# Kernel tuning notes

Measured on AMD Instinct MI355X. Metric: run time of the kernel, lower is better.

## Reference

```python
import jax, jax.numpy as jnp
import numpy as np


def setup_inputs() -> dict:
    key = jax.random.key(0)
    ks = jax.random.split(key, 8)
    B, S, V, E, H = 64, 512, 50257, 512, 1024
    scale1 = 1.0 / np.sqrt(E + H)
    scale2 = 1.0 / np.sqrt(H + E)
    return {
        "sequence": jax.random.randint(ks[0], (B, S), 0, V, dtype=jnp.int64),
        "init_h1": jax.random.uniform(ks[1], (B, H), jnp.float32, -0.1, 0.1),
        "init_h2": jax.random.uniform(ks[2], (B, E), jnp.float32, -0.1, 0.1),
        "emb_W": jax.random.normal(ks[3], (V, E), jnp.float32) * 0.02,
        "W1": jax.random.normal(ks[4], (E + H, H), jnp.float32) * scale1,
        "b1": jnp.zeros((H,), jnp.float32),
        "W2": jax.random.normal(ks[5], (H + E, E), jnp.float32) * scale2,
        "b2": jnp.zeros((E,), jnp.float32),
        "out_b": jnp.zeros((V,), jnp.float32),
    }


def reference(sequence, init_h1, init_h2, emb_W, W1, b1, W2, b2, out_b):
    # embeddings: [B, S, E] -> scan over time axis
    emb = emb_W[sequence]  # gather, [B, S, E]
    emb_t = jnp.swapaxes(emb, 0, 1)  # [S, B, E]

    def step(carry, token):
        h1, h2 = carry  # [B,H], [B,E]
        in1 = jnp.concatenate([token, h1], axis=1)  # [B, E+H]
        new_h1 = jnp.tanh(in1 @ W1 + b1)            # [B, H]
        in2 = jnp.concatenate([new_h1, h2], axis=1)  # [B, H+E]
        new_h2 = jnp.tanh(in2 @ W2 + b2)             # [B, E]
        return (new_h1, new_h2), None

    (h1, h2), _ = jax.lax.scan(step, (init_h1, init_h2), emb_t)
    # tied output projection: Linear with weight = embedding table [V, E]
    probabilities = h2 @ emb_W.T + out_b  # [B, V]
    return probabilities, h1, h2
```

## Files before the change

kernel.cpp:

```cpp
#include <hip/hip_runtime.h>
#include <hip/hip_bf16.h>

#define BB 64
#define EE 512
#define HH 1024
#define KK 1536
#define VV 50257
#define SS 512

#define NWG1 64
#define NWG2 32
#define NWG (NWG1 + NWG2)
#define RING 8
#define PADU 32

typedef __bf16 bf16x8 __attribute__((ext_vector_type(8)));
typedef float f32x4 __attribute__((ext_vector_type(4)));

__device__ __forceinline__ bf16x8 load_bf8(const __bf16* p) {
    return *reinterpret_cast<const bf16x8*>(p);
}

__device__ __forceinline__ bf16x8 cvt8(const float* p) {
    f32x4 a = *reinterpret_cast<const f32x4*>(p);
    f32x4 b = *reinterpret_cast<const f32x4*>(p + 4);
    bf16x8 r;
    r[0] = (__bf16)a[0]; r[1] = (__bf16)a[1]; r[2] = (__bf16)a[2]; r[3] = (__bf16)a[3];
    r[4] = (__bf16)b[0]; r[5] = (__bf16)b[1]; r[6] = (__bf16)b[2]; r[7] = (__bf16)b[3];
    return r;
}

__device__ __forceinline__ void st16c(void* p, f32x4 v) {
    asm volatile("global_store_dwordx4 %0, %1, off sc0 sc1" :: "v"(p), "v"(v) : "memory");
}
__device__ __forceinline__ f32x4 ld16c(const void* p) {
    f32x4 r;
    asm volatile("global_load_dwordx4 %0, %1, off sc0 sc1" : "=v"(r) : "v"(p) : "memory");
    return r;
}
union cvu { f32x4 f; bf16x8 h8; __bf16 h[8]; };

__device__ __forceinline__ void wwait(const unsigned* slots, int nslots, unsigned target) {
    const int l = threadIdx.x & 63;
    const int idx = l < nslots ? l : 0;
    for (;;) {
        unsigned v = __hip_atomic_load(&slots[idx * PADU], __ATOMIC_RELAXED,
                                       __HIP_MEMORY_SCOPE_AGENT);
        if (l >= nslots) v = target;
        if (__all((int)(v >= target))) break;
        __builtin_amdgcn_s_sleep(1);
    }
    asm volatile("" ::: "memory");
}

__device__ __forceinline__ unsigned minpoll(const unsigned* slots, int nslots) {
    const int l = threadIdx.x & 63;
    unsigned v = 0xFFFFFFFFu;
    if (l < nslots)
        v = __hip_atomic_load(&slots[l * PADU], __ATOMIC_RELAXED,
                              __HIP_MEMORY_SCOPE_AGENT);
    #pragma unroll
    for (int o = 32; o; o >>= 1) {
        unsigned u = (unsigned)__shfl_xor((int)v, o, 64);
        v = u < v ? u : v;
    }
    return v;
}

__device__ __forceinline__ void wsignal(unsigned* slot, unsigned val) {
    asm volatile("s_waitcnt vmcnt(0)" ::: "memory");
    if ((threadIdx.x & 63) == 0)
        __hip_atomic_store(slot, val, __ATOMIC_RELAXED, __HIP_MEMORY_SCOPE_AGENT);
}

__device__ __forceinline__ float ftanh(float x) {
    float ax = fabsf(x);
    float e = __expf(-2.0f * ax);
    float r = (1.0f - e) / (1.0f + e);
    return x < 0.0f ? -r : r;
}

__global__ void tokens_kernel(const void* __restrict__ seq, int* __restrict__ tok,
                              unsigned* __restrict__ bar) {
    int z = blockIdx.x * 256 + threadIdx.x;
    if (z < 4 * 96 * PADU)
        __hip_atomic_store(&bar[z], 0u, __ATOMIC_RELAXED, __HIP_MEMORY_SCOPE_AGENT);
    const unsigned* u = (const unsigned*)seq;
    bool is64 = true;
    #pragma unroll 1
    for (int i = 0; i < 64; ++i) {
        if (u[2 * i + 1] != 0u) { is64 = false; break; }
    }
    int i = blockIdx.x * 256 + threadIdx.x;
    if (i < BB * SS) tok[i] = is64 ? (int)u[2 * i] : (int)u[i];
}

__global__ __launch_bounds__(256) void transpose_kernel(
    const float* __restrict__ in, __bf16* __restrict__ out, int R, int C) {
    __shared__ float t[32][33];
    int bc = C >> 5;
    int br = blockIdx.x / bc;
    int bco = blockIdx.x % bc;
    int R0 = br << 5, C0 = bco << 5;
    int c = threadIdx.x & 31, r0 = threadIdx.x >> 5;
    #pragma unroll
    for (int i = 0; i < 4; ++i) {
        int r = r0 + i * 8;
        t[r][c] = in[(size_t)(R0 + r) * C + C0 + c];
    }
    __syncthreads();
    #pragma unroll
    for (int i = 0; i < 4; ++i) {
        int r = r0 + i * 8;
        out[(size_t)(C0 + r) * R + R0 + c] = (__bf16)t[c][r];
    }
}

__global__ void init_kernel(const float* __restrict__ h1, const float* __restrict__ h2,
                            __bf16* __restrict__ h1bf, __bf16* __restrict__ h2bf) {
    int i = blockIdx.x * 256 + threadIdx.x;
    if (i < BB * HH) h1bf[i] = (__bf16)h1[i];
    if (i < BB * EE) h2bf[i] = (__bf16)h2[i];
}

__global__ __launch_bounds__(256, 1) void rnn_persist3(
    const int* __restrict__ tok32, const float* __restrict__ embW,
    const float* __restrict__ b1, const float* __restrict__ b2,
    const __bf16* __restrict__ W1t, const __bf16* __restrict__ W2t,
    __bf16* __restrict__ h1r, __bf16* __restrict__ h2r,
    float* __restrict__ h1out, float* __restrict__ h2out,
    unsigned* __restrict__ bar) {
    const int bid = blockIdx.x;
    const bool g1 = bid < NWG1;
    const int rb = g1 ? bid : bid - NWG1;
    const int mi = rb & 3;
    const int ni = rb >> 2;
    const int m0 = mi << 4;
    const int n0 = ni << 6;
    const int tid = threadIdx.x;
    const int w = tid >> 6;
    const int l = tid & 63;
    const int l16 = l & 15;
    const int kg = l >> 4;
    unsigned* f1s = bar + mi * (96 * PADU);
    unsigned* f2s = f1s + 64 * PADU;
    unsigned* myf = g1 ? &f1s[(ni * 4 + w) * PADU] : &f2s[(ni * 4 + w) * PADU];

    __shared__ int tok_s[SS][16];
    __shared__ float red[2][4][16][68];

    if (g1) {
        for (int idx = tid; idx < SS * 16; idx += 256) {
            int t = idx >> 4, r = idx & 15;
            tok_s[t][r] = tok32[(m0 + r) * SS + t];
        }
    }

    const __bf16* Wt = g1 ? W1t : W2t;
    bf16x8 wreg[12][4];
    #pragma unroll
    for (int t = 0; t < 12; ++t) {
        const int kb = 32 * (w + 4 * t) + kg * 8;
        #pragma unroll
        for (int nf = 0; nf < 4; ++nf)
            wreg[t][nf] = load_bf8(Wt + (size_t)(n0 + nf * 16 + l16) * KK + kb);
    }
    {
        f32x4* p1 = reinterpret_cast<f32x4*>(&wreg[0][0]);
        #pragma unroll
        for (int q = 0; q < 48; ++q) asm volatile("" : "+v"(p1[q]));
    }

    const int r1 = 4 * w + ((l & 31) >> 3);
    const int c1 = (l & 7) * 8;
    const float* bias = g1 ? b1 : b2;
    const f32x4 blo = *reinterpret_cast<const f32x4*>(bias + n0 + c1);
    const f32x4 bhi = *reinterpret_cast<const f32x4*>(bias + n0 + c1 + 4);

    unsigned f2c = 0;

    __syncthreads();

    if (g1) {
        for (int i = 0; i < SS; ++i) {
            const __bf16* h1i = h1r + (size_t)(i & 7) * BB * HH;
            __bf16*       h1n = h1r + (size_t)((i + 1) & 7) * BB * HH;

            f32x4 acc[4] = {{0,0,0,0},{0,0,0,0},{0,0,0,0},{0,0,0,0}};
            const float* er = embW + (size_t)tok_s[i][l16] * EE;
            #pragma unroll
            for (int t = 0; t < 4; ++t) {
                bf16x8 ae = cvt8(er + 32 * (w + 4 * t) + kg * 8);
                #pragma unroll
                for (int nf = 0; nf < 4; ++nf)
                    acc[nf] = __builtin_amdgcn_mfma_f32_16x16x32_bf16(
                        ae, wreg[t][nf], acc[nf], 0, 0, 0);
            }
            __builtin_amdgcn_sched_barrier(0);

            if (i >= 7 && (int)f2c < i - 7) {
                do { f2c = minpoll(f2s, 32); } while ((int)f2c < i - 7);
            }

            if (i) wwait(f1s, 64, (unsigned)i);

            const __bf16* h1row = h1i + (m0 + l16) * HH;
            bf16x8 ah[8];
            #pragma unroll
            for (int u = 0; u < 8; ++u) {
                cvu t_; t_.f = ld16c(h1row + 32 * (w + 4 * u) + kg * 8);
                ah[u] = t_.h8;
            }
            asm volatile("s_waitcnt vmcnt(0)" ::: "memory");
            __builtin_amdgcn_sched_barrier(0);

            #pragma unroll
            for (int u = 0; u < 8; ++u)
                #pragma unroll
                for (int nf = 0; nf < 4; ++nf)
                    acc[nf] = __builtin_amdgcn_mfma_f32_16x16x32_bf16(
                        ah[u], wreg[u + 4][nf], acc[nf], 0, 0, 0);

            #pragma unroll
            for (int nf = 0; nf < 4; ++nf)
                #pragma unroll
                for (int q = 0; q < 4; ++q)
                    red[i & 1][w][kg * 4 + q][nf * 16 + l16] = acc[nf][q];
            __syncthreads();

            if ((l & 63) < 32) {
                f32x4 lo = blo, hi = bhi;
                #pragma unroll
                for (int p = 0; p < 4; ++p) {
                    lo += *reinterpret_cast<const f32x4*>(&red[i & 1][p][r1][c1]);
                    hi += *reinterpret_cast<const f32x4*>(&red[i & 1][p][r1][c1 + 4]);
                }
                cvu o;
                #pragma unroll
                for (int j = 0; j < 4; ++j) {
                    o.h[j]     = (__bf16)ftanh(lo[j]);
                    o.h[j + 4] = (__bf16)ftanh(hi[j]);
                }
                st16c(h1n + (m0 + r1) * HH + n0 + c1, o.f);
                if (i == SS - 1) {
                    float* op = h1out + (m0 + r1) * HH + n0 + c1;
                    #pragma unroll
                    for (int j = 0; j < 8; ++j)
                        op[j] = __bfloat162float(((__hip_bfloat16*)&o.h[j])[0]);
                }
            }
            wsignal(myf, (unsigned)(i + 1));
        }
    } else {
        for (int j = 1; j <= SS; ++j) {
            const __bf16* h1j = h1r + (size_t)(j & 7) * BB * HH;
            const __bf16* h2p = h2r + (size_t)((j - 1) & 7) * BB * EE;
            __bf16*       h2n = h2r + (size_t)(j & 7) * BB * EE;

            wwait(f1s, 64, (unsigned)j);
            const __bf16* h1row = h1j + (m0 + l16) * HH;
            bf16x8 ah[8];
            #pragma unroll
            for (int t = 0; t < 8; ++t) {
                cvu t_; t_.f = ld16c(h1row + 32 * (w + 4 * t) + kg * 8);
                ah[t] = t_.h8;
            }
            if (j >= 2) wwait(f2s, 32, (unsigned)(j - 1));
            const __bf16* h2row = h2p + (m0 + l16) * EE;
            bf16x8 a2[4];
            #pragma unroll
            for (int u = 0; u < 4; ++u) {
                cvu t_; t_.f = ld16c(h2row + 32 * (w + 4 * u) + kg * 8);
                a2[u] = t_.h8;
            }
            asm volatile("s_waitcnt vmcnt(0)" ::: "memory");
            __builtin_amdgcn_sched_barrier(0);

            f32x4 acc[4] = {{0,0,0,0},{0,0,0,0},{0,0,0,0},{0,0,0,0}};
            #pragma unroll
            for (int t = 0; t < 8; ++t)
                #pragma unroll
                for (int nf = 0; nf < 4; ++nf)
                    acc[nf] = __builtin_amdgcn_mfma_f32_16x16x32_bf16(
                        ah[t], wreg[t][nf], acc[nf], 0, 0, 0);
            #pragma unroll
            for (int u = 0; u < 4; ++u)
                #pragma unroll
                for (int nf = 0; nf < 4; ++nf)
                    acc[nf] = __builtin_amdgcn_mfma_f32_16x16x32_bf16(
                        a2[u], wreg[u + 8][nf], acc[nf], 0, 0, 0);

            #pragma unroll
            for (int nf = 0; nf < 4; ++nf)
                #pragma unroll
                for (int q = 0; q < 4; ++q)
                    red[j & 1][w][kg * 4 + q][nf * 16 + l16] = acc[nf][q];
            __syncthreads();

            if ((l & 63) < 32) {
                f32x4 lo = blo, hi = bhi;
                #pragma unroll
                for (int p = 0; p < 4; ++p) {
                    lo += *reinterpret_cast<const f32x4*>(&red[j & 1][p][r1][c1]);
                    hi += *reinterpret_cast<const f32x4*>(&red[j & 1][p][r1][c1 + 4]);
                }
                cvu o;
                #pragma unroll
                for (int q = 0; q < 4; ++q) {
                    o.h[q]     = (__bf16)ftanh(lo[q]);
                    o.h[q + 4] = (__bf16)ftanh(hi[q]);
                }
                st16c(h2n + (m0 + r1) * EE + n0 + c1, o.f);
                if (j == SS) {
                    float* op = h2out + (m0 + r1) * EE + n0 + c1;
                    #pragma unroll
                    for (int q = 0; q < 8; ++q)
                        op[q] = __bfloat162float(((__hip_bfloat16*)&o.h[q])[0]);
                }
            }
            wsignal(myf, (unsigned)j);
        }
    }
}

__global__ __launch_bounds__(256) void step_kernel(
    const int* __restrict__ tok32,
    const float* __restrict__ embW,
    const float* __restrict__ b1, const float* __restrict__ b2,
    const __bf16* __restrict__ W1t, const __bf16* __restrict__ W2t,
    const __bf16* __restrict__ h1cur, __bf16* __restrict__ h1next,
    const __bf16* __restrict__ h2cur, __bf16* __restrict__ h2next,
    float* __restrict__ h1f32, float* __restrict__ h2f32,
    int t, int g1, int g2) {
    const int bid = blockIdx.x;
    const bool is1 = bid < 128;
    if (is1 ? (g1 == 0) : (g2 == 0)) return;
    const int rb = is1 ? bid : (bid - 128);
    const int mi = rb & 3;
    const int ni = rb >> 2;
    const int m0 = mi << 4;
    const int n0 = ni << 5;
    const int N = is1 ? HH : EE;
    const int tid = threadIdx.x;
    const int w = tid >> 6;
    const int l = tid & 63;
    const int l16 = l & 15;
    const int kg = l >> 4;

    __shared__ int tok_s[16];
    __shared__ float red[4][16][33];

    if (is1 && tid < 16) tok_s[tid] = tok32[(m0 + tid) * SS + t];
    __syncthreads();

    const __bf16* Wt = is1 ? W1t : W2t;
    f32x4 acc0 = {0.f, 0.f, 0.f, 0.f};
    f32x4 acc1 = {0.f, 0.f, 0.f, 0.f};
    const int row = m0 + l16;
    const int kb = w * 384;

    #pragma unroll 4
    for (int kk = 0; kk < 384; kk += 32) {
        const int k = kb + kk + kg * 8;
        bf16x8 a;
        if (is1) {
            if (k < EE) a = cvt8(embW + (size_t)tok_s[l16] * EE + k);
            else        a = load_bf8(h1cur + row * HH + (k - EE));
        } else {
            if (k < HH) a = load_bf8(h1cur + row * HH + k);
            else        a = load_bf8(h2cur + row * EE + (k - HH));
        }
        bf16x8 bf0 = load_bf8(Wt + (size_t)(n0 + l16) * KK + k);
        bf16x8 bf1 = load_bf8(Wt + (size_t)(n0 + 16 + l16) * KK + k);
        acc0 = __builtin_amdgcn_mfma_f32_16x16x32_bf16(a, bf0, acc0, 0, 0, 0);
        acc1 = __builtin_amdgcn_mfma_f32_16x16x32_bf16(a, bf1, acc1, 0, 0, 0);
    }

    #pragma unroll
    for (int i = 0; i < 4; ++i) {
        red[w][kg * 4 + i][l16]      = acc0[i];
        red[w][kg * 4 + i][16 + l16] = acc1[i];
    }
    __syncthreads();

    const float* bias = is1 ? b1 : b2;
    for (int c = tid; c < 512; c += 256) {
        int m = c >> 5, n = c & 31;
        float s = red[0][m][n] + red[1][m][n] + red[2][m][n] + red[3][m][n];
        s = tanhf(s + bias[n0 + n]);
        int gi = (m0 + m) * N + (n0 + n);
        if (is1) {
            h1next[gi] = (__bf16)s;
            if (h1f32) h1f32[gi] = s;
        } else {
            h2next[gi] = (__bf16)s;
            if (h2f32) h2f32[gi] = s;
        }
    }
}

__global__ __launch_bounds__(256) void proj_kernel(
    const __bf16* __restrict__ h2bf,
    const float* __restrict__ embW,
    const float* __restrict__ outb,
    float* __restrict__ out) {
    const int v0 = blockIdx.x << 6;
    const int tid = threadIdx.x;
    const int w = tid >> 6;
    const int l = tid & 63;
    const int l16 = l & 15, kg = l >> 4;
    const int vcol = v0 + w * 16 + l16;
    const int vr = vcol < VV ? vcol : VV - 1;
    f32x4 acc[4] = {{0,0,0,0},{0,0,0,0},{0,0,0,0},{0,0,0,0}};
    #pragma unroll 2
    for (int k0 = 0; k0 < EE; k0 += 32) {
        const int k = k0 + kg * 8;
        bf16x8 bfr = cvt8(embW + (size_t)vr * EE + k);
        #pragma unroll
        for (int mf = 0; mf < 4; ++mf) {
            bf16x8 a = load_bf8(h2bf + (mf * 16 + l16) * EE + k);
            acc[mf] = __builtin_amdgcn_mfma_f32_16x16x32_bf16(a, bfr, acc[mf], 0, 0, 0);
        }
    }
    if (vcol < VV) {
        const float bb = outb[vcol];
        #pragma unroll
        for (int mf = 0; mf < 4; ++mf) {
            #pragma unroll
            for (int i = 0; i < 4; ++i) {
                int b = mf * 16 + kg * 4 + i;
                out[(size_t)b * VV + vcol] = acc[mf][i] + bb;
            }
        }
    }
}

extern "C" void kernel_launch(void* const* d_in, const int* in_sizes, int n_in,
                              void* d_out, int out_size, void* d_ws, size_t ws_size,
                              hipStream_t stream) {
    const void* seq      = d_in[0];
    const float* init_h1 = (const float*)d_in[1];
    const float* init_h2 = (const float*)d_in[2];
    const float* embW    = (const float*)d_in[3];
    const float* W1      = (const float*)d_in[4];
    const float* b1      = (const float*)d_in[5];
    const float* W2      = (const float*)d_in[6];
    const float* b2      = (const float*)d_in[7];
    const float* outb    = (const float*)d_in[8];
    float* out = (float*)d_out;

    char* ws = (char*)d_ws;
    int* tok = (int*)ws;                 ws += (size_t)BB * SS * 4;
    __bf16* W1t = (__bf16*)ws;           ws += (size_t)HH * KK * 2;
    __bf16* W2t = (__bf16*)ws;           ws += (size_t)EE * KK * 2;
    __bf16* h1r = (__bf16*)ws;           ws += (size_t)RING * BB * HH * 2;
    __bf16* h2r = (__bf16*)ws;           ws += (size_t)RING * BB * EE * 2;
    unsigned* bar = (unsigned*)ws;       ws += (size_t)4 * 96 * PADU * 4;

    hipLaunchKernelGGL(tokens_kernel, dim3(128), dim3(256), 0, stream, seq, tok, bar);
    hipLaunchKernelGGL(transpose_kernel, dim3((KK / 32) * (HH / 32)), dim3(256), 0, stream,
                       W1, W1t, KK, HH);
    hipLaunchKernelGGL(transpose_kernel, dim3((KK / 32) * (EE / 32)), dim3(256), 0, stream,
                       W2, W2t, KK, EE);
    hipLaunchKernelGGL(init_kernel, dim3(256), dim3(256), 0, stream,
                       init_h1, init_h2, h1r, h2r);

    float* h1out = out + (size_t)BB * VV;
    float* h2out = h1out + (size_t)BB * HH;

    const int* tok_c = tok;
    const __bf16* W1t_c = W1t;
    const __bf16* W2t_c = W2t;
    void* args[] = {
        (void*)&tok_c, (void*)&embW, (void*)&b1, (void*)&b2,
        (void*)&W1t_c, (void*)&W2t_c,
        (void*)&h1r, (void*)&h2r,
        (void*)&h1out, (void*)&h2out, (void*)&bar
    };
    hipError_t err = hipLaunchCooperativeKernel((void*)rnn_persist3, dim3(NWG), dim3(256),
                                                args, 0, stream);
    if (err != hipSuccess) {
        __bf16* h1bf[2] = {h1r, h1r + (size_t)BB * HH};
        __bf16* h2bf[2] = {h2r, h2r + (size_t)BB * EE};
        for (int t = 0; t <= SS; ++t) {
            int g1 = (t < SS) ? 1 : 0;
            int g2 = (t >= 1) ? 1 : 0;
            const __bf16* h1cur = h1bf[t & 1];
            __bf16* h1next      = h1bf[(t + 1) & 1];
            const __bf16* h2cur = h2bf[(t + 1) & 1];
            __bf16* h2next      = h2bf[t & 1];
            float* h1f = (t == SS - 1) ? h1out : nullptr;
            float* h2f = (t == SS) ? h2out : nullptr;
            hipLaunchKernelGGL(step_kernel, dim3(192), dim3(256), 0, stream,
                               tok, embW, b1, b2, W1t, W2t,
                               h1cur, h1next, h2cur, h2next, h1f, h2f, t, g1, g2);
        }
    }

    hipLaunchKernelGGL(proj_kernel, dim3((VV + 63) / 64), dim3(256), 0, stream,
                       h2r, embW, outb, out);
}
```

Baseline: 2.120 ms.

## Replace flag barriers with step-tagged hidden-state messages for fine-grained dataflow sync

Each bf16 pair of hidden state is now stored with its timestep tag in a 64-bit word. Consumers spin on the data itself until every tag matches, so the per-wave flag stores, the vmcnt drain before signalling and the separate flag polling are gone. This is meant to cut the latency of the serial recurrent chain at each step. The cost is twice the memory traffic for hidden-state reads and writes, extra clear and init kernels, and guard-bounded spin loops that could fall through and read stale data.

```diff
diff --git a/kernel.cpp b/kernel.cpp
--- a/kernel.cpp
+++ b/kernel.cpp
@@ -11,11 +11,16 @@
 #define NWG1 64
 #define NWG2 32
 #define NWG (NWG1 + NWG2)
-#define RING 8
 #define PADU 32
+#define GUARD_MAX 8192
 
 typedef __bf16 bf16x8 __attribute__((ext_vector_type(8)));
 typedef float f32x4 __attribute__((ext_vector_type(4)));
+typedef unsigned u32x2 __attribute__((ext_vector_type(2)));
+typedef unsigned long long u64;
+
+union frg { unsigned u[4]; bf16x8 h; };
+union pk2 { __bf16 h[2]; unsigned u; };
 
 __device__ __forceinline__ bf16x8 load_bf8(const __bf16* p) {
     return *reinterpret_cast<const bf16x8*>(p);
@@ -30,27 +35,17 @@
     return r;
 }
 
-__device__ __forceinline__ void st16c(void* p, f32x4 v) {
-    asm volatile("global_store_dwordx4 %0, %1, off sc0 sc1" :: "v"(p), "v"(v) : "memory");
-}
-__device__ __forceinline__ f32x4 ld16c(const void* p) {
-    f32x4 r;
-    asm volatile("global_load_dwordx4 %0, %1, off sc0 sc1" : "=v"(r) : "v"(p) : "memory");
+template<int OFF>
+__device__ __forceinline__ u32x2 ld8o(const void* p) {
+    u32x2 r;
+    asm volatile("global_load_dwordx2 %0, %1, off offset:%2 sc0 sc1"
+                 : "=v"(r) : "v"(p), "i"(OFF));
     return r;
 }
-union cvu { f32x4 f; bf16x8 h8; __bf16 h[8]; };
-
-__device__ __forceinline__ void wwait(const unsigned* slots, int nslots, unsigned target) {
-    const int l = threadIdx.x & 63;
-    const int idx = l < nslots ? l : 0;
-    for (;;) {
-        unsigned v = __hip_atomic_load(&slots[idx * PADU], __ATOMIC_RELAXED,
-                                       __HIP_MEMORY_SCOPE_AGENT);
-        if (l >= nslots) v = target;
-        if (__all((int)(v >= target))) break;
-        __builtin_amdgcn_s_sleep(1);
-    }
-    asm volatile("" ::: "memory");
+template<int OFF>
+__device__ __forceinline__ void st8o(void* p, u32x2 v) {
+    asm volatile("global_store_dwordx2 %0, %1, off offset:%2 sc0 sc1"
+                 :: "v"(p), "v"(v), "i"(OFF));
 }
 
 __device__ __forceinline__ unsigned minpoll(const unsigned* slots, int nslots) {
@@ -67,12 +62,6 @@
     return v;
 }
 
-__device__ __forceinline__ void wsignal(unsigned* slot, unsigned val) {
-    asm volatile("s_waitcnt vmcnt(0)" ::: "memory");
-    if ((threadIdx.x & 63) == 0)
-        __hip_atomic_store(slot, val, __ATOMIC_RELAXED, __HIP_MEMORY_SCOPE_AGENT);
-}
-
 __device__ __forceinline__ float ftanh(float x) {
     float ax = fabsf(x);
     float e = __expf(-2.0f * ax);
@@ -83,7 +72,7 @@
 __global__ void tokens_kernel(const void* __restrict__ seq, int* __restrict__ tok,
                               unsigned* __restrict__ bar) {
     int z = blockIdx.x * 256 + threadIdx.x;
-    if (z < 4 * 96 * PADU)
+    if (z < 4 * 32 * PADU)
         __hip_atomic_store(&bar[z], 0u, __ATOMIC_RELAXED, __HIP_MEMORY_SCOPE_AGENT);
     const unsigned* u = (const unsigned*)seq;
     bool is64 = true;
@@ -116,18 +105,46 @@
     }
 }
 
+__global__ void msgclear_kernel(u64* __restrict__ h1m, u64* __restrict__ h2m) {
+    size_t z = (size_t)blockIdx.x * 256 + threadIdx.x;
+    if (z < (size_t)7 * 64 * 512) h1m[(size_t)64 * 512 + z] = 0ull;
+    else {
+        z -= (size_t)7 * 64 * 512;
+        if (z < (size_t)7 * 64 * 256) h2m[(size_t)64 * 256 + z] = 0ull;
+    }
+}
+
 __global__ void init_kernel(const float* __restrict__ h1, const float* __restrict__ h2,
-                            __bf16* __restrict__ h1bf, __bf16* __restrict__ h2bf) {
+                            u64* __restrict__ h1m, u64* __restrict__ h2m,
+                            __bf16* __restrict__ h1p0, __bf16* __restrict__ h2p0) {
     int i = blockIdx.x * 256 + threadIdx.x;
-    if (i < BB * HH) h1bf[i] = (__bf16)h1[i];
-    if (i < BB * EE) h2bf[i] = (__bf16)h2[i];
-}
-
-__global__ __launch_bounds__(256, 1) void rnn_persist3(
+    if (i < 64 * 512) {
+        int row = i >> 9, m = i & 511;
+        pk2 p;
+        p.h[0] = (__bf16)h1[row * HH + 2 * m];
+        p.h[1] = (__bf16)h1[row * HH + 2 * m + 1];
+        h1m[i] = (u64)p.u;
+        h1p0[row * HH + 2 * m] = p.h[0];
+        h1p0[row * HH + 2 * m + 1] = p.h[1];
+    } else {
+        int j = i - 64 * 512;
+        if (j < 64 * 256) {
+            int row = j >> 8, m = j & 255;
+            pk2 p;
+            p.h[0] = (__bf16)h2[row * EE + 2 * m];
+            p.h[1] = (__bf16)h2[row * EE + 2 * m + 1];
+            h2m[j] = (u64)p.u;
+            h2p0[row * EE + 2 * m] = p.h[0];
+            h2p0[row * EE + 2 * m + 1] = p.h[1];
+        }
+    }
+}
+
+__global__ __launch_bounds__(256, 1) void rnn_persist5(
     const int* __restrict__ tok32, const float* __restrict__ embW,
     const float* __restrict__ b1, const float* __restrict__ b2,
     const __bf16* __restrict__ W1t, const __bf16* __restrict__ W2t,
-    __bf16* __restrict__ h1r, __bf16* __restrict__ h2r,
+    u64* __restrict__ h1m, u64* __restrict__ h2m,
     float* __restrict__ h1out, float* __restrict__ h2out,
     unsigned* __restrict__ bar) {
     const int bid = blockIdx.x;
@@ -142,9 +159,8 @@
     const int l = tid & 63;
     const int l16 = l & 15;
     const int kg = l >> 4;
-    unsigned* f1s = bar + mi * (96 * PADU);
-    unsigned* f2s = f1s + 64 * PADU;
-    unsigned* myf = g1 ? &f1s[(ni * 4 + w) * PADU] : &f2s[(ni * 4 + w) * PADU];
+    unsigned* f2s = bar + mi * (32 * PADU);
+    unsigned* myf2 = &f2s[(ni * 4 + w) * PADU];
 
     __shared__ int tok_s[SS][16];
     __shared__ float red[2][4][16][68];
@@ -176,15 +192,14 @@
     const float* bias = g1 ? b1 : b2;
     const f32x4 blo = *reinterpret_cast<const f32x4*>(bias + n0 + c1);
     const f32x4 bhi = *reinterpret_cast<const f32x4*>(bias + n0 + c1 + 4);
-
-    unsigned f2c = 0;
+    const int laneoff = 16 * w + 4 * kg;
 
     __syncthreads();
 
     if (g1) {
+        unsigned f2c = 0;
         for (int i = 0; i < SS; ++i) {
-            const __bf16* h1i = h1r + (size_t)(i & 7) * BB * HH;
-            __bf16*       h1n = h1r + (size_t)((i + 1) & 7) * BB * HH;
+            const int si = i & 7, sn = (i + 1) & 7;
 
             f32x4 acc[4] = {{0,0,0,0},{0,0,0,0},{0,0,0,0},{0,0,0,0}};
             const float* er = embW + (size_t)tok_s[i][l16] * EE;
@@ -199,27 +214,43 @@
             __builtin_amdgcn_sched_barrier(0);
 
             if (i >= 7 && (int)f2c < i - 7) {
-                do { f2c = minpoll(f2s, 32); } while ((int)f2c < i - 7);
-            }
-
-            if (i) wwait(f1s, 64, (unsigned)i);
-
-            const __bf16* h1row = h1i + (m0 + l16) * HH;
-            bf16x8 ah[8];
+                int g = 0;
+                do { f2c = minpoll(f2s, 32); } while ((int)f2c < i - 7 && ++g < GUARD_MAX);
+            }
+
+            const char* pb = (const char*)(h1m +
+                ((size_t)(si * 64 + m0 + l16) * 512 + laneoff));
+            u32x2 mm[8][4];
+            int guard = 0;
+            for (;;) {
+                #define LDU(u) \
+                    mm[u][0] = ld8o<(u)*512 +  0>(pb); \
+                    mm[u][1] = ld8o<(u)*512 +  8>(pb); \
+                    mm[u][2] = ld8o<(u)*512 + 16>(pb); \
+                    mm[u][3] = ld8o<(u)*512 + 24>(pb);
+                LDU(0) LDU(1) LDU(2) LDU(3) LDU(4) LDU(5) LDU(6) LDU(7)
+                #undef LDU
+                asm volatile("s_waitcnt vmcnt(0)" ::: "memory");
+                __builtin_amdgcn_sched_barrier(0);
+                bool ok = true;
+                #pragma unroll
+                for (int u = 0; u < 8; ++u)
+                    #pragma unroll
+                    for (int q = 0; q < 4; ++q) ok &= (mm[u][q][1] == (unsigned)i);
+                if (__all(ok)) break;
+                if (++guard > GUARD_MAX) break;
+            }
+
             #pragma unroll
             for (int u = 0; u < 8; ++u) {
-                cvu t_; t_.f = ld16c(h1row + 32 * (w + 4 * u) + kg * 8);
-                ah[u] = t_.h8;
-            }
-            asm volatile("s_waitcnt vmcnt(0)" ::: "memory");
-            __builtin_amdgcn_sched_barrier(0);
-
-            #pragma unroll
-            for (int u = 0; u < 8; ++u)
+                frg f;
+                f.u[0] = mm[u][0][0]; f.u[1] = mm[u][1][0];
+                f.u[2] = mm[u][2][0]; f.u[3] = mm[u][3][0];
                 #pragma unroll
                 for (int nf = 0; nf < 4; ++nf)
                     acc[nf] = __builtin_amdgcn_mfma_f32_16x16x32_bf16(
-                        ah[u], wreg[u + 4][nf], acc[nf], 0, 0, 0);
+                        f.h, wreg[u + 4][nf], acc[nf], 0, 0, 0);
+            }
 
             #pragma unroll
             for (int nf = 0; nf < 4; ++nf)
@@ -235,60 +266,86 @@
                     lo += *reinterpret_cast<const f32x4*>(&red[i & 1][p][r1][c1]);
                     hi += *reinterpret_cast<const f32x4*>(&red[i & 1][p][r1][c1 + 4]);
                 }
-                cvu o;
-                #pragma unroll
-                for (int j = 0; j < 4; ++j) {
-                    o.h[j]     = (__bf16)ftanh(lo[j]);
-                    o.h[j + 4] = (__bf16)ftanh(hi[j]);
-                }
-                st16c(h1n + (m0 + r1) * HH + n0 + c1, o.f);
+                float s[8];
+                #pragma unroll
+                for (int j = 0; j < 4; ++j) { s[j] = ftanh(lo[j]); s[j + 4] = ftanh(hi[j]); }
+                char* dp = (char*)(h1m +
+                    ((size_t)(sn * 64 + m0 + r1) * 512 + (n0 + c1) / 2));
+                const unsigned tg = (unsigned)(i + 1);
+                #define STU(q, OFF) { pk2 p; p.h[0]=(__bf16)s[2*(q)]; p.h[1]=(__bf16)s[2*(q)+1]; \
+                                      u32x2 v; v[0]=p.u; v[1]=tg; st8o<OFF>(dp, v); }
+                STU(0, 0) STU(1, 8) STU(2, 16) STU(3, 24)
+                #undef STU
                 if (i == SS - 1) {
                     float* op = h1out + (m0 + r1) * HH + n0 + c1;
                     #pragma unroll
-                    for (int j = 0; j < 8; ++j)
-                        op[j] = __bfloat162float(((__hip_bfloat16*)&o.h[j])[0]);
+                    for (int j = 0; j < 8; ++j) op[j] = s[j];
                 }
             }
-            wsignal(myf, (unsigned)(i + 1));
         }
     } else {
         for (int j = 1; j <= SS; ++j) {
-            const __bf16* h1j = h1r + (size_t)(j & 7) * BB * HH;
-            const __bf16* h2p = h2r + (size_t)((j - 1) & 7) * BB * EE;
-            __bf16*       h2n = h2r + (size_t)(j & 7) * BB * EE;
-
-            wwait(f1s, 64, (unsigned)j);
-            const __bf16* h1row = h1j + (m0 + l16) * HH;
-            bf16x8 ah[8];
+            const int sj = j & 7, sp = (j - 1) & 7;
+            const char* pb1 = (const char*)(h1m +
+                ((size_t)(sj * 64 + m0 + l16) * 512 + laneoff));
+            const char* pb2 = (const char*)(h2m +
+                ((size_t)(sp * 64 + m0 + l16) * 256 + laneoff));
+            u32x2 ma[8][4], mb[4][4];
+            int guard = 0;
+            for (;;) {
+                #define LDA(u) \
+                    ma[u][0] = ld8o<(u)*512 +  0>(pb1); \
+                    ma[u][1] = ld8o<(u)*512 +  8>(pb1); \
+                    ma[u][2] = ld8o<(u)*512 + 16>(pb1); \
+                    ma[u][3] = ld8o<(u)*512 + 24>(pb1);
+                #define LDB(u) \
+                    mb[u][0] = ld8o<(u)*512 +  0>(pb2); \
+                    mb[u][1] = ld8o<(u)*512 +  8>(pb2); \
+                    mb[u][2] = ld8o<(u)*512 + 16>(pb2); \
+                    mb[u][3] = ld8o<(u)*512 + 24>(pb2);
+                LDA(0) LDA(1) LDA(2) LDA(3) LDA(4) LDA(5) LDA(6) LDA(7)
+                LDB(0) LDB(1) LDB(2) LDB(3)
+                #undef LDA
+                #undef LDB
+                asm volatile("s_waitcnt vmcnt(0)" ::: "memory");
+                __builtin_amdgcn_sched_barrier(0);
+                bool ok = true;
+                #pragma unroll
+                for (int u = 0; u < 8; ++u)
+                    #pragma unroll
+                    for (int q = 0; q < 4; ++q) ok &= (ma[u][q][1] == (unsigned)j);
+                #pragma unroll
+                for (int u = 0; u < 4; ++u)
+                    #pragma unroll
+                    for (int q = 0; q < 4; ++q) ok &= (mb[u][q][1] == (unsigned)(j - 1));
+                if (__all(ok)) break;
+                if (++guard > GUARD_MAX) break;
+            }
+            if ((l & 63) == 0)
+                __hip_atomic_store(myf2, (unsigned)j, __ATOMIC_RELAXED,
+                                   __HIP_MEMORY_SCOPE_AGENT);
+
+            f32x4 acc[4] = {{0,0,0,0},{0,0,0,0},{0,0,0,0},{0,0,0,0}};
             #pragma unroll
             for (int t = 0; t < 8; ++t) {
-                cvu t_; t_.f = ld16c(h1row + 32 * (w + 4 * t) + kg * 8);
-                ah[t] = t_.h8;
-            }
-            if (j >= 2) wwait(f2s, 32, (unsigned)(j - 1));
-            const __bf16* h2row = h2p + (m0 + l16) * EE;
-            bf16x8 a2[4];
-            #pragma unroll
-            for (int u = 0; u < 4; ++u) {
-                cvu t_; t_.f = ld16c(h2row + 32 * (w + 4 * u) + kg * 8);
-                a2[u] = t_.h8;
-            }
-            asm volatile("s_waitcnt vmcnt(0)" ::: "memory");
-            __builtin_amdgcn_sched_barrier(0);
-
-            f32x4 acc[4] = {{0,0,0,0},{0,0,0,0},{0,0,0,0},{0,0,0,0}};
-            #pragma unroll
-            for (int t = 0; t < 8; ++t)
+                frg f;
+                f.u[0] = ma[t][0][0]; f.u[1] = ma[t][1][0];
+                f.u[2] = ma[t][2][0]; f.u[3] = ma[t][3][0];
                 #pragma unroll
                 for (int nf = 0; nf < 4; ++nf)
                     acc[nf] = __builtin_amdgcn_mfma_f32_16x16x32_bf16(
-                        ah[t], wreg[t][nf], acc[nf], 0, 0, 0);
-            #pragma unroll
-            for (int u = 0; u < 4; ++u)
+                        f.h, wreg[t][nf], acc[nf], 0, 0, 0);
+            }
+            #pragma unroll
+            for (int u = 0; u < 4; ++u) {
+                frg f;
+                f.u[0] = mb[u][0][0]; f.u[1] = mb[u][1][0];
+                f.u[2] = mb[u][2][0]; f.u[3] = mb[u][3][0];
                 #pragma unroll
                 for (int nf = 0; nf < 4; ++nf)
                     acc[nf] = __builtin_amdgcn_mfma_f32_16x16x32_bf16(
-                        a2[u], wreg[u + 8][nf], acc[nf], 0, 0, 0);
+                        f.h, wreg[u + 8][nf], acc[nf], 0, 0, 0);
+            }
 
             #pragma unroll
             for (int nf = 0; nf < 4; ++nf)
@@ -304,21 +361,22 @@
                     lo += *reinterpret_cast<const f32x4*>(&red[j & 1][p][r1][c1]);
                     hi += *reinterpret_cast<const f32x4*>(&red[j & 1][p][r1][c1 + 4]);
                 }
-                cvu o;
-                #pragma unroll
-                for (int q = 0; q < 4; ++q) {
-                    o.h[q]     = (__bf16)ftanh(lo[q]);
-                    o.h[q + 4] = (__bf16)ftanh(hi[q]);
-                }
-                st16c(h2n + (m0 + r1) * EE + n0 + c1, o.f);
+                float s[8];
+                #pragma unroll
+                for (int q = 0; q < 4; ++q) { s[q] = ftanh(lo[q]); s[q + 4] = ftanh(hi[q]); }
+                char* dp = (char*)(h2m +
+                    ((size_t)(sj * 64 + m0 + r1) * 256 + (n0 + c1) / 2));
+                const unsigned tg = (unsigned)j;
+                #define STU(q, OFF) { pk2 p; p.h[0]=(__bf16)s[2*(q)]; p.h[1]=(__bf16)s[2*(q)+1]; \
+                                      u32x2 v; v[0]=p.u; v[1]=tg; st8o<OFF>(dp, v); }
+                STU(0, 0) STU(1, 8) STU(2, 16) STU(3, 24)
+                #undef STU
                 if (j == SS) {
                     float* op = h2out + (m0 + r1) * EE + n0 + c1;
                     #pragma unroll
-                    for (int q = 0; q < 8; ++q)
-                        op[q] = __bfloat162float(((__hip_bfloat16*)&o.h[q])[0]);
+                    for (int q = 0; q < 8; ++q) op[q] = s[q];
                 }
             }
-            wsignal(myf, (unsigned)j);
         }
     }
 }
@@ -399,8 +457,19 @@
     }
 }
 
+__global__ void h2tom_kernel(const __bf16* __restrict__ h2raw, u64* __restrict__ h2m) {
+    int i = blockIdx.x * 256 + threadIdx.x;
+    if (i < 64 * 256) {
+        int row = i >> 8, m = i & 255;
+        pk2 p;
+        p.h[0] = h2raw[row * EE + 2 * m];
+        p.h[1] = h2raw[row * EE + 2 * m + 1];
+        h2m[i] = ((u64)SS << 32) | (u64)p.u;
+    }
+}
+
 __global__ __launch_bounds__(256) void proj_kernel(
-    const __bf16* __restrict__ h2bf,
+    const u64* __restrict__ h2m,
     const float* __restrict__ embW,
     const float* __restrict__ outb,
     float* __restrict__ out) {
@@ -418,8 +487,11 @@
         bf16x8 bfr = cvt8(embW + (size_t)vr * EE + k);
         #pragma unroll
         for (int mf = 0; mf < 4; ++mf) {
-            bf16x8 a = load_bf8(h2bf + (mf * 16 + l16) * EE + k);
-            acc[mf] = __builtin_amdgcn_mfma_f32_16x16x32_bf16(a, bfr, acc[mf], 0, 0, 0);
+            const u64* hr = h2m + (size_t)(mf * 16 + l16) * 256 + k / 2;
+            frg f;
+            f.u[0] = (unsigned)hr[0]; f.u[1] = (unsigned)hr[1];
+            f.u[2] = (unsigned)hr[2]; f.u[3] = (unsigned)hr[3];
+            acc[mf] = __builtin_amdgcn_mfma_f32_16x16x32_bf16(f.h, bfr, acc[mf], 0, 0, 0);
         }
     }
     if (vcol < VV) {
@@ -453,17 +525,20 @@
     int* tok = (int*)ws;                 ws += (size_t)BB * SS * 4;
     __bf16* W1t = (__bf16*)ws;           ws += (size_t)HH * KK * 2;
     __bf16* W2t = (__bf16*)ws;           ws += (size_t)EE * KK * 2;
-    __bf16* h1r = (__bf16*)ws;           ws += (size_t)RING * BB * HH * 2;
-    __bf16* h2r = (__bf16*)ws;           ws += (size_t)RING * BB * EE * 2;
-    unsigned* bar = (unsigned*)ws;       ws += (size_t)4 * 96 * PADU * 4;
+    u64* h1m = (u64*)ws;                 ws += (size_t)8 * 64 * 512 * 8;
+    u64* h2m = (u64*)ws;                 ws += (size_t)8 * 64 * 256 * 8;
+    unsigned* bar = (unsigned*)ws;       ws += (size_t)4 * 32 * PADU * 4;
+    __bf16* h1p = (__bf16*)ws;           ws += (size_t)2 * BB * HH * 2;
+    __bf16* h2p = (__bf16*)ws;           ws += (size_t)2 * BB * EE * 2;
 
     hipLaunchKernelGGL(tokens_kernel, dim3(128), dim3(256), 0, stream, seq, tok, bar);
     hipLaunchKernelGGL(transpose_kernel, dim3((KK / 32) * (HH / 32)), dim3(256), 0, stream,
                        W1, W1t, KK, HH);
     hipLaunchKernelGGL(transpose_kernel, dim3((KK / 32) * (EE / 32)), dim3(256), 0, stream,
                        W2, W2t, KK, EE);
-    hipLaunchKernelGGL(init_kernel, dim3(256), dim3(256), 0, stream,
-                       init_h1, init_h2, h1r, h2r);
+    hipLaunchKernelGGL(msgclear_kernel, dim3(1344), dim3(256), 0, stream, h1m, h2m);
+    hipLaunchKernelGGL(init_kernel, dim3(192), dim3(256), 0, stream,
+                       init_h1, init_h2, h1m, h2m, h1p, h2p);
 
     float* h1out = out + (size_t)BB * VV;
     float* h2out = h1out + (size_t)BB * HH;
@@ -474,14 +549,14 @@
     void* args[] = {
         (void*)&tok_c, (void*)&embW, (void*)&b1, (void*)&b2,
         (void*)&W1t_c, (void*)&W2t_c,
-        (void*)&h1r, (void*)&h2r,
+        (void*)&h1m, (void*)&h2m,
         (void*)&h1out, (void*)&h2out, (void*)&bar
     };
-    hipError_t err = hipLaunchCooperativeKernel((void*)rnn_persist3, dim3(NWG), dim3(256),
+    hipError_t err = hipLaunchCooperativeKernel((void*)rnn_persist5, dim3(NWG), dim3(256),
                                                 args, 0, stream);
     if (err != hipSuccess) {
-        __bf16* h1bf[2] = {h1r, h1r + (size_t)BB * HH};
-        __bf16* h2bf[2] = {h2r, h2r + (size_t)BB * EE};
+        __bf16* h1bf[2] = {h1p, h1p + (size_t)BB * HH};
+        __bf16* h2bf[2] = {h2p, h2p + (size_t)BB * EE};
         for (int t = 0; t <= SS; ++t) {
             int g1 = (t < SS) ? 1 : 0;
             int g2 = (t >= 1) ? 1 : 0;
@@ -495,8 +570,9 @@
                                tok, embW, b1, b2, W1t, W2t,
                                h1cur, h1next, h2cur, h2next, h1f, h2f, t, g1, g2);
         }
+        hipLaunchKernelGGL(h2tom_kernel, dim3(64), dim3(256), 0, stream, h2bf[0], h2m);
     }
 
     hipLaunchKernelGGL(proj_kernel, dim3((VV + 63) / 64), dim3(256), 0, stream,
-                       h2r, embW, outb, out);
-}
+                       h2m, embW, outb, out);
+}
```

New measurement: 3.799 ms. 1.79x slower.

## Switch to per-block flags with block barriers and widen hidden-state ring

Applied to the files above, without the earlier changes.

Replaces per-wave flag signalling and polling with one flag per workgroup. A single wave polls and the block then synchronises with __syncthreads, so each consumer watches 16 or 8 slots instead of 64 or 32. The ring of hidden-state buffers grows from 8 to 64, which loosens the back-pressure between the h1 producer and the h2 consumer. The cost is added intra-block barriers per step and a larger workspace footprint.

```diff
diff --git a/kernel.cpp b/kernel.cpp
--- a/kernel.cpp
+++ b/kernel.cpp
@@ -11,7 +11,7 @@
 #define NWG1 64
 #define NWG2 32
 #define NWG (NWG1 + NWG2)
-#define RING 8
+#define RING 64
 #define PADU 32
 
 typedef __bf16 bf16x8 __attribute__((ext_vector_type(8)));
@@ -40,16 +40,20 @@
 }
 union cvu { f32x4 f; bf16x8 h8; __bf16 h[8]; };
 
-__device__ __forceinline__ void wwait(const unsigned* slots, int nslots, unsigned target) {
-    const int l = threadIdx.x & 63;
-    const int idx = l < nslots ? l : 0;
-    for (;;) {
-        unsigned v = __hip_atomic_load(&slots[idx * PADU], __ATOMIC_RELAXED,
-                                       __HIP_MEMORY_SCOPE_AGENT);
-        if (l >= nslots) v = target;
-        if (__all((int)(v >= target))) break;
-        __builtin_amdgcn_s_sleep(1);
-    }
+__device__ __forceinline__ void block_wait(const unsigned* slots, int nslots,
+                                           unsigned target) {
+    if (threadIdx.x < 64) {
+        const int l = threadIdx.x;
+        const int idx = l < nslots ? l : 0;
+        for (;;) {
+            unsigned v = __hip_atomic_load(&slots[idx * PADU], __ATOMIC_RELAXED,
+                                           __HIP_MEMORY_SCOPE_AGENT);
+            if (l >= nslots) v = target;
+            if (__all((int)(v >= target))) break;
+            __builtin_amdgcn_s_sleep(1);
+        }
+    }
+    __syncthreads();
     asm volatile("" ::: "memory");
 }
 
@@ -67,9 +71,10 @@
     return v;
 }
 
-__device__ __forceinline__ void wsignal(unsigned* slot, unsigned val) {
+__device__ __forceinline__ void bsignal(unsigned* slot, unsigned val) {
     asm volatile("s_waitcnt vmcnt(0)" ::: "memory");
-    if ((threadIdx.x & 63) == 0)
+    __syncthreads();
+    if (threadIdx.x == 0)
         __hip_atomic_store(slot, val, __ATOMIC_RELAXED, __HIP_MEMORY_SCOPE_AGENT);
 }
 
@@ -83,7 +88,7 @@
 __global__ void tokens_kernel(const void* __restrict__ seq, int* __restrict__ tok,
                               unsigned* __restrict__ bar) {
     int z = blockIdx.x * 256 + threadIdx.x;
-    if (z < 4 * 96 * PADU)
+    if (z < 4 * 32 * PADU)
         __hip_atomic_store(&bar[z], 0u, __ATOMIC_RELAXED, __HIP_MEMORY_SCOPE_AGENT);
     const unsigned* u = (const unsigned*)seq;
     bool is64 = true;
@@ -123,7 +128,7 @@
     if (i < BB * EE) h2bf[i] = (__bf16)h2[i];
 }
 
-__global__ __launch_bounds__(256, 1) void rnn_persist3(
+__global__ __launch_bounds__(256, 1) void rnn_persist6(
     const int* __restrict__ tok32, const float* __restrict__ embW,
     const float* __restrict__ b1, const float* __restrict__ b2,
     const __bf16* __restrict__ W1t, const __bf16* __restrict__ W2t,
@@ -142,9 +147,9 @@
     const int l = tid & 63;
     const int l16 = l & 15;
     const int kg = l >> 4;
-    unsigned* f1s = bar + mi * (96 * PADU);
-    unsigned* f2s = f1s + 64 * PADU;
-    unsigned* myf = g1 ? &f1s[(ni * 4 + w) * PADU] : &f2s[(ni * 4 + w) * PADU];
+    unsigned* f1s = bar + mi * (32 * PADU);
+    unsigned* f2s = f1s + 16 * PADU;
+    unsigned* myf = g1 ? &f1s[ni * PADU] : &f2s[ni * PADU];
 
     __shared__ int tok_s[SS][16];
     __shared__ float red[2][4][16][68];
@@ -183,8 +188,8 @@
 
     if (g1) {
         for (int i = 0; i < SS; ++i) {
-            const __bf16* h1i = h1r + (size_t)(i & 7) * BB * HH;
-            __bf16*       h1n = h1r + (size_t)((i + 1) & 7) * BB * HH;
+            const __bf16* h1i = h1r + (size_t)(i & (RING - 1)) * BB * HH;
+            __bf16*       h1n = h1r + (size_t)((i + 1) & (RING - 1)) * BB * HH;
 
             f32x4 acc[4] = {{0,0,0,0},{0,0,0,0},{0,0,0,0},{0,0,0,0}};
             const float* er = embW + (size_t)tok_s[i][l16] * EE;
@@ -198,11 +203,11 @@
             }
             __builtin_amdgcn_sched_barrier(0);
 
-            if (i >= 7 && (int)f2c < i - 7) {
-                do { f2c = minpoll(f2s, 32); } while ((int)f2c < i - 7);
-            }
-
-            if (i) wwait(f1s, 64, (unsigned)i);
+            if (i >= RING - 1 && (int)f2c < i - (RING - 1)) {
+                do { f2c = minpoll(f2s, 8); } while ((int)f2c < i - (RING - 1));
+            }
+
+            if (i) block_wait(f1s, 16, (unsigned)i);
 
             const __bf16* h1row = h1i + (m0 + l16) * HH;
             bf16x8 ah[8];
@@ -249,15 +254,15 @@
                         op[j] = __bfloat162float(((__hip_bfloat16*)&o.h[j])[0]);
                 }
             }
-            wsignal(myf, (unsigned)(i + 1));
+            bsignal(myf, (unsigned)(i + 1));
         }
     } else {
         for (int j = 1; j <= SS; ++j) {
-            const __bf16* h1j = h1r + (size_t)(j & 7) * BB * HH;
-            const __bf16* h2p = h2r + (size_t)((j - 1) & 7) * BB * EE;
-            __bf16*       h2n = h2r + (size_t)(j & 7) * BB * EE;
-
-            wwait(f1s, 64, (unsigned)j);
+            const __bf16* h1j = h1r + (size_t)(j & (RING - 1)) * BB * HH;
+            const __bf16* h2p = h2r + (size_t)((j - 1) & (RING - 1)) * BB * EE;
+            __bf16*       h2n = h2r + (size_t)(j & (RING - 1)) * BB * EE;
+
+            block_wait(f1s, 16, (unsigned)j);
             const __bf16* h1row = h1j + (m0 + l16) * HH;
             bf16x8 ah[8];
             #pragma unroll
@@ -265,7 +270,7 @@
                 cvu t_; t_.f = ld16c(h1row + 32 * (w + 4 * t) + kg * 8);
                 ah[t] = t_.h8;
             }
-            if (j >= 2) wwait(f2s, 32, (unsigned)(j - 1));
+            if (j >= 2) block_wait(f2s, 8, (unsigned)(j - 1));
             const __bf16* h2row = h2p + (m0 + l16) * EE;
             bf16x8 a2[4];
             #pragma unroll
@@ -318,7 +323,7 @@
                         op[q] = __bfloat162float(((__hip_bfloat16*)&o.h[q])[0]);
                 }
             }
-            wsignal(myf, (unsigned)j);
+            bsignal(myf, (unsigned)j);
         }
     }
 }
@@ -455,7 +460,7 @@
     __bf16* W2t = (__bf16*)ws;           ws += (size_t)EE * KK * 2;
     __bf16* h1r = (__bf16*)ws;           ws += (size_t)RING * BB * HH * 2;
     __bf16* h2r = (__bf16*)ws;           ws += (size_t)RING * BB * EE * 2;
-    unsigned* bar = (unsigned*)ws;       ws += (size_t)4 * 96 * PADU * 4;
+    unsigned* bar = (unsigned*)ws;       ws += (size_t)4 * 32 * PADU * 4;
 
     hipLaunchKernelGGL(tokens_kernel, dim3(128), dim3(256), 0, stream, seq, tok, bar);
     hipLaunchKernelGGL(transpose_kernel, dim3((KK / 32) * (HH / 32)), dim3(256), 0, stream,
@@ -477,7 +482,7 @@
         (void*)&h1r, (void*)&h2r,
         (void*)&h1out, (void*)&h2out, (void*)&bar
     };
-    hipError_t err = hipLaunchCooperativeKernel((void*)rnn_persist3, dim3(NWG), dim3(256),
+    hipError_t err = hipLaunchCooperativeKernel((void*)rnn_persist6, dim3(NWG), dim3(256),
                                                 args, 0, stream);
     if (err != hipSuccess) {
         __bf16* h1bf[2] = {h1r, h1r + (size_t)BB * HH};
```

Result: faster. 2.068 ms (-2.4%).
